# Optimization experiments

Hardware: AMD Instinct MI355X
Metric: run time of the kernel (lower is better)

Reference implementation:

```python
import jax, jax.numpy as jnp
import numpy as np

LSH_NUM_PROJS = 7
BLOCK_SIZE = 256      # key block size
SAMPLE_SIZE = 256
B, H, N, D = 1, 32, 8192, 128


def _gray_perm(num_projs):
    # AngularLSH._unit_hamming_distance_array: Gray-code bucket permutation
    a = np.array([0, 1], dtype=np.int32)
    for _ in range(num_projs - 1):
        a = np.concatenate([a, np.flip(a) + a.shape[0]])
    return jnp.asarray(a)


def _lsh_hash(x, proj_dir, perm):
    # x: [B,H,N,D], proj_dir: [D,R] -> bucket ids [B,H,N]
    bits = jnp.einsum('bhnd,dr->bhnr', x, proj_dir) > 0
    enc = 2 ** jnp.arange(proj_dir.shape[-1], dtype=jnp.int32)
    bin_ids = jnp.sum(bits.astype(jnp.int32) * enc, axis=-1)
    return perm[bin_ids]


def _attn_lse(q, k, v, scale, bias=None):
    # exact attention returning output and log-sum-exp of scaled scores
    s = jnp.einsum('...qd,...kd->...qk', q, k) * scale
    if bias is not None:
        s = s + bias
    m = jnp.max(s, axis=-1, keepdims=True)
    p = jnp.exp(s - m)
    denom = jnp.sum(p, axis=-1, keepdims=True)
    attn = jnp.einsum('...qk,...kd->...qd', p, v) / denom
    lse = m + jnp.log(denom)  # [..., q, 1]
    return attn, lse


def _take(x, idx):
    # gather along the sequence axis (dim 2); idx: [B,H,M]
    return jnp.take_along_axis(x, idx[..., None], axis=2)


def hyper_attention(q, k, v, proj_dir, sampled_set):
    b, h, n, d = q.shape
    scale = d ** -0.5
    perm = _gray_perm(LSH_NUM_PROJS)
    # 1) sortLSH: sort q and k by angular-LSH bucket (stable)
    q_idx = jnp.argsort(_lsh_hash(q, proj_dir, perm), axis=2)
    k_idx = jnp.argsort(_lsh_hash(k, proj_dir, perm), axis=2)
    q_idx_inv = jnp.argsort(q_idx, axis=2)
    q_s = _take(q, q_idx)
    k_s = _take(k, k_idx)
    v_s = _take(v, k_idx)
    nb = n // BLOCK_SIZE          # number of key blocks
    qbs = n // nb                 # query block size
    # block-diagonal exact attention in sorted order
    qb = q_s.reshape(b, h, nb, qbs, d)
    kb = k_s.reshape(b, h, nb, BLOCK_SIZE, d)
    vb = v_s.reshape(b, h, nb, BLOCK_SIZE, d)
    attn_blk, lse_blk = _attn_lse(qb, kb, vb, scale)
    attn_blk = attn_blk.reshape(b, h, n, d)
    lse_blk = lse_blk.reshape(b, h, n, 1)
    attn_blk = _take(attn_blk, q_idx_inv)
    lse_blk = _take(lse_blk, q_idx_inv)
    # 2) residual: uniform sampling of keys (indices into sorted key order)
    s_size = sampled_set.shape[-1]
    k_sub = _take(k_s, sampled_set)   # [B,H,S,D]
    v_sub = _take(v_s, sampled_set)
    # mask out samples falling in the query's own diagonal block
    same_block = (jnp.arange(n)[None, None, :, None] // qbs) == (sampled_set[:, :, None, :] // BLOCK_SIZE)
    bias = jnp.where(same_block, jnp.finfo(q.dtype).min, 0.0).astype(q.dtype)
    attn_res, lse_res = _attn_lse(q_s, k_sub, v_sub, scale, bias=bias)
    lse_res = lse_res + jnp.log(n / s_size)  # importance weight n_key/sample_size
    attn_res = _take(attn_res, q_idx_inv)
    lse_res = _take(lse_res, q_idx_inv)
    # 3) combine estimators: softmax-weighted average in log space
    lse = jnp.logaddexp(lse_blk, lse_res)
    return jnp.exp(lse_blk - lse) * attn_blk + jnp.exp(lse_res - lse) * attn_res


def setup_inputs() -> dict:
    key = jax.random.key(0)
    k1, k2, k3, k4, k5 = jax.random.split(key, 5)
    return {
        'queries': jax.random.normal(k1, (B, H, N, D), dtype=jnp.float32),
        'keys': jax.random.normal(k2, (B, H, N, D), dtype=jnp.float32),
        'vals': jax.random.normal(k3, (B, H, N, D), dtype=jnp.float32),
        'proj_dir': jax.random.normal(k4, (D, LSH_NUM_PROJS), dtype=jnp.float32),
        'sampled_set': jax.random.randint(k5, (B, H, SAMPLE_SIZE), 0, N),
    }


def reference(queries, keys, vals, proj_dir, sampled_set):
    return hyper_attention(queries, keys, vals, proj_dir, sampled_set)
```

## Files before the change

kernel.cpp:

```cpp
#include <hip/hip_runtime.h>
#include <hip/hip_bf16.h>
#include <math.h>

#define Hh 32
#define Nseq 8192
#define Dh 128
#define NBd 32
#define BLKSZ 256
#define SAMP 256
#define CHK 64
#define NCH 8
#define LOG32 3.4657359027997265f
#define SCALE 0.088388347648318447f
#define SKW 136
#define SVW 72

typedef float f32x4 __attribute__((ext_vector_type(4)));
typedef unsigned ui32x4 __attribute__((ext_vector_type(4)));
typedef __bf16 bf16x8 __attribute__((ext_vector_type(8)));

__device__ __forceinline__ f32x4 mfma16(bf16x8 a, bf16x8 b, f32x4 c) {
  return __builtin_amdgcn_mfma_f32_16x16x32_bf16(a, b, c, 0, 0, 0);
}

__device__ __forceinline__ bf16x8 cvt8(const float* __restrict__ p) {
  float4 a = ((const float4*)p)[0];
  float4 b = ((const float4*)p)[1];
  bf16x8 r;
  r[0] = (__bf16)a.x; r[1] = (__bf16)a.y; r[2] = (__bf16)a.z; r[3] = (__bf16)a.w;
  r[4] = (__bf16)b.x; r[5] = (__bf16)b.y; r[6] = (__bf16)b.z; r[7] = (__bf16)b.w;
  return r;
}

__device__ __forceinline__ bf16x8 cvt8v(float4 a, float4 b) {
  bf16x8 r;
  r[0] = (__bf16)a.x; r[1] = (__bf16)a.y; r[2] = (__bf16)a.z; r[3] = (__bf16)a.w;
  r[4] = (__bf16)b.x; r[5] = (__bf16)b.y; r[6] = (__bf16)b.z; r[7] = (__bf16)b.w;
  return r;
}

__device__ __forceinline__ unsigned packv(float a, float b) {
  __bf16 ba = (__bf16)a, bb = (__bf16)b;
  return ((unsigned)__builtin_bit_cast(unsigned short, bb) << 16) |
         (unsigned)__builtin_bit_cast(unsigned short, ba);
}

__device__ __forceinline__ unsigned pack2(float a, float b, float& ra, float& rb) {
  __bf16 ba = (__bf16)a, bb = (__bf16)b;
  ra = (float)ba; rb = (float)bb;
  return ((unsigned)__builtin_bit_cast(unsigned short, bb) << 16) |
         (unsigned)__builtin_bit_cast(unsigned short, ba);
}

__global__ __launch_bounds__(256) void lsh_hash_kernel(
    const float* __restrict__ q, const float* __restrict__ k,
    const float* __restrict__ proj, int* __restrict__ buckets) {
  int row = blockIdx.x * 256 + threadIdx.x;
  const float* x = ((row >> 18) ? k : q) + (size_t)(row & (Hh * Nseq - 1)) * Dh;
  double acc[7] = {0, 0, 0, 0, 0, 0, 0};
#pragma unroll 8
  for (int d0 = 0; d0 < Dh; d0 += 4) {
    float4 xv = *(const float4*)(x + d0);
    double x0 = (double)xv.x, x1 = (double)xv.y, x2 = (double)xv.z, x3 = (double)xv.w;
#pragma unroll
    for (int j = 0; j < 7; j++) {
      acc[j] = fma(x0, (double)proj[(d0 + 0) * 7 + j], acc[j]);
      acc[j] = fma(x1, (double)proj[(d0 + 1) * 7 + j], acc[j]);
      acc[j] = fma(x2, (double)proj[(d0 + 2) * 7 + j], acc[j]);
      acc[j] = fma(x3, (double)proj[(d0 + 3) * 7 + j], acc[j]);
    }
  }
  int bin = 0;
#pragma unroll
  for (int j = 0; j < 7; j++) bin |= (acc[j] > 0.0 ? 1 : 0) << j;
  buckets[row] = bin ^ (bin >> 1);
}

__global__ __launch_bounds__(256) void bucket_sort_kernel(
    const int* __restrict__ buckets, int* __restrict__ idx) {
  __shared__ unsigned short hist[256][128];
  __shared__ unsigned btot[128];
  __shared__ unsigned wsum[2];
  const int t = threadIdx.x;
  const int base = blockIdx.x * Nseq;

  {
    uint4* h4 = (uint4*)&hist[0][0];
#pragma unroll
    for (int j = 0; j < 16; j++) h4[t + j * 256] = uint4{0, 0, 0, 0};
  }
  __syncthreads();

  int bloc[32];
#pragma unroll 8
  for (int i = 0; i < 32; i++) {
    int b = buckets[base + t * 32 + i];
    bloc[i] = b;
    hist[t][b]++;
  }
  __syncthreads();

  unsigned v = 0;
  if (t < 128) {
    unsigned run = 0;
    for (int cch = 0; cch < 256; cch++) {
      unsigned h = hist[cch][t];
      hist[cch][t] = (unsigned short)run;
      run += h;
    }
    btot[t] = run;
    v = run;
  }
  __syncthreads();

  unsigned sc = v;
  if (t < 128) {
#pragma unroll
    for (int s = 1; s < 64; s <<= 1) {
      unsigned u = __shfl_up(sc, s);
      if ((t & 63) >= s) sc += u;
    }
    if ((t & 63) == 63) wsum[t >> 6] = sc;
  }
  __syncthreads();
  if (t < 128) {
    unsigned excl = sc - v + ((t >> 6) ? wsum[0] : 0u);
    btot[t] = excl;
  }
  __syncthreads();
  if (t < 128) {
    unsigned short e = (unsigned short)btot[t];
    for (int cch = 0; cch < 256; cch++) hist[cch][t] += e;
  }
  __syncthreads();

#pragma unroll 8
  for (int i = 0; i < 32; i++) {
    int b = bloc[i];
    unsigned pos = hist[t][b]++;
    idx[base + pos] = t * 32 + i;
  }
}

__global__ __launch_bounds__(256) void permute_samp_kernel(
    const float* __restrict__ k, const float* __restrict__ v,
    const int* __restrict__ k_idx, const int* __restrict__ sampled,
    __bf16* __restrict__ K_sp, __bf16* __restrict__ V_sp) {
  __shared__ __attribute__((aligned(16))) __bf16 s_t[Dh][SVW];
  const int tile = blockIdx.x, bh = blockIdx.y;
  const int t = threadIdx.x;
  const int j = t >> 2, seg = (t & 3) * 32;
  const int dpos = tile * 64 + j;
  const int sp = sampled[bh * SAMP + dpos];
  const int orig = k_idx[bh * Nseq + sp];
  {
    const float4* kp = (const float4*)(k + ((size_t)bh * Nseq + orig) * Dh + seg);
    __bf16* dst = K_sp + ((size_t)bh * SAMP + dpos) * Dh + seg;
#pragma unroll
    for (int i = 0; i < 4; i++) *(bf16x8*)(dst + i * 8) = cvt8v(kp[2 * i], kp[2 * i + 1]);
  }
  {
    const float4* vp = (const float4*)(v + ((size_t)bh * Nseq + orig) * Dh + seg);
#pragma unroll
    for (int i = 0; i < 8; i++) {
      float4 a = vp[i];
      s_t[seg + i * 4 + 0][j] = (__bf16)a.x;
      s_t[seg + i * 4 + 1][j] = (__bf16)a.y;
      s_t[seg + i * 4 + 2][j] = (__bf16)a.z;
      s_t[seg + i * 4 + 3][j] = (__bf16)a.w;
    }
  }
  __syncthreads();
  {
    int d = t >> 1, half = (t & 1) * 32;
    __bf16* dst = V_sp + ((size_t)(bh * Dh + d)) * SAMP + tile * 64 + half;
    const __bf16* srcp = &s_t[d][half];
#pragma unroll
    for (int i = 0; i < 4; i++) *(ui32x4*)(dst + i * 8) = *(const ui32x4*)(srcp + i * 8);
  }
}

__global__ __launch_bounds__(512, 2) void hyper_attn_kernel(
    const float* __restrict__ q, const float* __restrict__ k, const float* __restrict__ v,
    const __bf16* __restrict__ K_sp, const __bf16* __restrict__ V_sp,
    const int* __restrict__ sampled, const int* __restrict__ q_idx,
    const int* __restrict__ k_idx, float* __restrict__ out) {
  __shared__ int s_orig[BLKSZ];
  __shared__ __attribute__((aligned(16))) float s_add[SAMP];
  __shared__ __attribute__((aligned(16))) __bf16 s_k[2][CHK][SKW];
  __shared__ __attribute__((aligned(16))) __bf16 s_vt[2][Dh][SVW];

  const int c = blockIdx.x, bh = blockIdx.y;
  const int tid = threadIdx.x;
  const int w = tid >> 6, l = tid & 63;
  const int l4 = l >> 4, lm = l & 15;
  const int jk = tid >> 3, pk = tid & 7;
  const int dv = tid >> 2, ks = (tid & 3) * 16;
  const int kb = (tid & 31) * 2, dg = tid >> 5;

  {
    int jj = tid;
    if (jj < BLKSZ) {
      s_orig[jj] = k_idx[bh * Nseq + c * BLKSZ + jj];
    } else {
      int sp = sampled[bh * SAMP + (jj - BLKSZ)];
      s_add[jj - BLKSZ] = ((sp >> 8) == c) ? -1e38f : LOG32;
    }
  }

  bf16x8 qf[2][4];
  const int* qi = q_idx + bh * Nseq + c * BLKSZ + w * 32;
#pragma unroll
  for (int rt = 0; rt < 2; rt++) {
    int orig = qi[rt * 16 + lm];
    const float* qp = q + ((size_t)bh * Nseq + orig) * Dh + l4 * 8;
#pragma unroll
    for (int dc = 0; dc < 4; dc++) qf[rt][dc] = cvt8(qp + dc * 32);
  }

  f32x4 O[2][8];
  float mrow[2] = {-INFINITY, -INFINITY};
  float lsum[2] = {0.f, 0.f};
#pragma unroll
  for (int rt = 0; rt < 2; rt++)
#pragma unroll
    for (int dt = 0; dt < 8; dt++) { O[rt][dt][0]=0.f; O[rt][dt][1]=0.f; O[rt][dt][2]=0.f; O[rt][dt][3]=0.f; }

  __syncthreads();

  {
    int origk = s_orig[jk];
    const float* kp = k + ((size_t)bh * Nseq + origk) * Dh + pk * 16;
    *(bf16x8*)&s_k[0][jk][pk * 16]     = cvt8(kp);
    *(bf16x8*)&s_k[0][jk][pk * 16 + 8] = cvt8(kp + 8);
    int ra = s_orig[kb], rb = s_orig[kb + 1];
    const float4* va = (const float4*)(v + ((size_t)bh * Nseq + ra) * Dh + dg * 8);
    const float4* vb = (const float4*)(v + ((size_t)bh * Nseq + rb) * Dh + dg * 8);
    float4 A0 = va[0], A1 = va[1], B0 = vb[0], B1 = vb[1];
    float ta[8] = {A0.x,A0.y,A0.z,A0.w,A1.x,A1.y,A1.z,A1.w};
    float tb[8] = {B0.x,B0.y,B0.z,B0.w,B1.x,B1.y,B1.z,B1.w};
#pragma unroll
    for (int dd = 0; dd < 8; dd++)
      *(unsigned*)&s_vt[0][dg * 8 + dd][kb] = packv(ta[dd], tb[dd]);
  }
  __syncthreads();

  const int laneA = lm + 32 * (l4 & 1);
  const bool hi = (l4 >> 1) & 1;

  for (int ch = 0; ch < NCH; ch++) {
    const int cur = ch & 1;
    const int cn = ch + 1;
    const bool pfg = (cn < 4);
    const bool pfc = (cn >= 4 && cn < NCH);

    float4 kA, kB, kC, kD, vA0, vA1, vB0, vB1;
    ui32x4 ksA, ksB, vsA, vsB;
    if (pfg) {
      int origk = s_orig[cn * CHK + jk];
      const float4* kp = (const float4*)(k + ((size_t)bh * Nseq + origk) * Dh + pk * 16);
      kA = kp[0]; kB = kp[1]; kC = kp[2]; kD = kp[3];
      int ra = s_orig[cn * CHK + kb], rb = s_orig[cn * CHK + kb + 1];
      const float4* va = (const float4*)(v + ((size_t)bh * Nseq + ra) * Dh + dg * 8);
      const float4* vb = (const float4*)(v + ((size_t)bh * Nseq + rb) * Dh + dg * 8);
      vA0 = va[0]; vA1 = va[1]; vB0 = vb[0]; vB1 = vb[1];
    } else if (pfc) {
      const __bf16* kp = K_sp + ((size_t)(bh * SAMP + (cn - 4) * CHK + jk)) * Dh + pk * 16;
      ksA = *(const ui32x4*)kp; ksB = *(const ui32x4*)(kp + 8);
      const __bf16* vp = V_sp + ((size_t)(bh * Dh + dv)) * SAMP + (cn - 4) * CHK + ks;
      vsA = *(const ui32x4*)vp; vsB = *(const ui32x4*)(vp + 8);
    }
    __builtin_amdgcn_sched_barrier(0);

    float sc[2][4][4];
    __builtin_amdgcn_s_setprio(1);
#pragma unroll
    for (int ct = 0; ct < 4; ct++) {
      f32x4 acc0, acc1;
      acc0[0]=0.f;acc0[1]=0.f;acc0[2]=0.f;acc0[3]=0.f;
      acc1[0]=0.f;acc1[1]=0.f;acc1[2]=0.f;acc1[3]=0.f;
#pragma unroll
      for (int dc = 0; dc < 4; dc++) {
        bf16x8 kf = *(const bf16x8*)&s_k[cur][ct * 16 + lm][dc * 32 + l4 * 8];
        acc0 = mfma16(kf, qf[0][dc], acc0);
        acc1 = mfma16(kf, qf[1][dc], acc1);
      }
      f32x4 addv;
      if (ch < 4) { addv[0]=0.f; addv[1]=0.f; addv[2]=0.f; addv[3]=0.f; }
      else addv = *(const f32x4*)&s_add[(ch - 4) * CHK + ct * 16 + l4 * 4];
#pragma unroll
      for (int r = 0; r < 4; r++) {
        sc[0][ct][r] = acc0[r] * SCALE + addv[r];
        sc[1][ct][r] = acc1[r] * SCALE + addv[r];
      }
    }
    __builtin_amdgcn_s_setprio(0);

    unsigned q01[2][4], q23[2][4];
#pragma unroll
    for (int rt = 0; rt < 2; rt++) {
      float mc = sc[rt][0][0];
#pragma unroll
      for (int ct = 0; ct < 4; ct++)
#pragma unroll
        for (int r = 0; r < 4; r++) mc = fmaxf(mc, sc[rt][ct][r]);
      mc = fmaxf(mc, __shfl_xor(mc, 16));
      mc = fmaxf(mc, __shfl_xor(mc, 32));
      float mn = fmaxf(mrow[rt], mc);
      float alpha = __expf(mrow[rt] - mn);
      mrow[rt] = mn;
      f32x4 aO;
#pragma unroll
      for (int r = 0; r < 4; r++) aO[r] = __shfl(alpha, l4 * 4 + r);
#pragma unroll
      for (int dt = 0; dt < 8; dt++) O[rt][dt] *= aO;
      float rsum = 0.f;
#pragma unroll
      for (int ct = 0; ct < 4; ct++) {
        float p0 = __expf(sc[rt][ct][0] - mn);
        float p1 = __expf(sc[rt][ct][1] - mn);
        float p2 = __expf(sc[rt][ct][2] - mn);
        float p3 = __expf(sc[rt][ct][3] - mn);
        float ra, rb, rc, rd;
        q01[rt][ct] = pack2(p0, p1, ra, rb);
        q23[rt][ct] = pack2(p2, p3, rc, rd);
        rsum += (ra + rb) + (rc + rd);
      }
      rsum += __shfl_xor(rsum, 16);
      rsum += __shfl_xor(rsum, 32);
      lsum[rt] = lsum[rt] * alpha + rsum;
    }

    if (pfg) {
      *(bf16x8*)&s_k[cur ^ 1][jk][pk * 16]     = cvt8v(kA, kB);
      *(bf16x8*)&s_k[cur ^ 1][jk][pk * 16 + 8] = cvt8v(kC, kD);
      float ta[8] = {vA0.x,vA0.y,vA0.z,vA0.w,vA1.x,vA1.y,vA1.z,vA1.w};
      float tb[8] = {vB0.x,vB0.y,vB0.z,vB0.w,vB1.x,vB1.y,vB1.z,vB1.w};
#pragma unroll
      for (int dd = 0; dd < 8; dd++)
        *(unsigned*)&s_vt[cur ^ 1][dg * 8 + dd][kb] = packv(ta[dd], tb[dd]);
    } else if (pfc) {
      *(ui32x4*)&s_k[cur ^ 1][jk][pk * 16]     = ksA;
      *(ui32x4*)&s_k[cur ^ 1][jk][pk * 16 + 8] = ksB;
      *(ui32x4*)&s_vt[cur ^ 1][dv][ks]     = vsA;
      *(ui32x4*)&s_vt[cur ^ 1][dv][ks + 8] = vsB;
    }

    __builtin_amdgcn_s_setprio(1);
#pragma unroll
    for (int kc = 0; kc < 2; kc++) {
      bf16x8 pa[2];
#pragma unroll
      for (int rt = 0; rt < 2; rt++) {
        unsigned a0 = __shfl((int)q01[rt][2 * kc],     laneA);
        unsigned b0 = __shfl((int)q01[rt][2 * kc + 1], laneA);
        unsigned a1 = __shfl((int)q23[rt][2 * kc],     laneA);
        unsigned b1 = __shfl((int)q23[rt][2 * kc + 1], laneA);
        unsigned a2 = __shfl((int)q01[rt][2 * kc],     laneA + 16);
        unsigned b2 = __shfl((int)q01[rt][2 * kc + 1], laneA + 16);
        unsigned a3 = __shfl((int)q23[rt][2 * kc],     laneA + 16);
        unsigned b3 = __shfl((int)q23[rt][2 * kc + 1], laneA + 16);
        ui32x4 pw;
        pw[0] = hi ? b0 : a0;
        pw[1] = hi ? b1 : a1;
        pw[2] = hi ? b2 : a2;
        pw[3] = hi ? b3 : a3;
        pa[rt] = __builtin_bit_cast(bf16x8, pw);
      }
#pragma unroll
      for (int dt = 0; dt < 8; dt++) {
        bf16x8 vb = *(const bf16x8*)&s_vt[cur][dt * 16 + lm][kc * 32 + l4 * 8];
        O[0][dt] = mfma16(pa[0], vb, O[0][dt]);
        O[1][dt] = mfma16(pa[1], vb, O[1][dt]);
      }
    }
    __builtin_amdgcn_s_setprio(0);
    __syncthreads();
  }

#pragma unroll
  for (int rt = 0; rt < 2; rt++) {
    float inv = 1.0f / lsum[rt];
    f32x4 invr;
#pragma unroll
    for (int r = 0; r < 4; r++) invr[r] = __shfl(inv, l4 * 4 + r);
#pragma unroll
    for (int r = 0; r < 4; r++) {
      int orow = q_idx[bh * Nseq + c * BLKSZ + w * 32 + rt * 16 + l4 * 4 + r];
      float* op = out + ((size_t)bh * Nseq + orow) * Dh + lm;
#pragma unroll
      for (int dt = 0; dt < 8; dt++) op[dt * 16] = O[rt][dt][r] * invr[r];
    }
  }
}

extern "C" void kernel_launch(void* const* d_in, const int* in_sizes, int n_in,
                              void* d_out, int out_size, void* d_ws, size_t ws_size,
                              hipStream_t stream) {
  const float* q    = (const float*)d_in[0];
  const float* k    = (const float*)d_in[1];
  const float* v    = (const float*)d_in[2];
  const float* proj = (const float*)d_in[3];
  const int* samp   = (const int*)d_in[4];
  float* out = (float*)d_out;

  int* buckets = (int*)d_ws;
  int* idx = buckets + 2 * Hh * Nseq;
  __bf16* K_sp = (__bf16*)(idx + 2 * Hh * Nseq);
  __bf16* V_sp = K_sp + (size_t)Hh * SAMP * Dh;

  lsh_hash_kernel<<<(2 * Hh * Nseq) / 256, 256, 0, stream>>>(q, k, proj, buckets);
  bucket_sort_kernel<<<2 * Hh, 256, 0, stream>>>(buckets, idx);
  permute_samp_kernel<<<dim3(4, Hh), 256, 0, stream>>>(
      k, v, idx + Hh * Nseq , samp, K_sp, V_sp);
  hyper_attn_kernel<<<dim3(NBd, Hh), 512, 0, stream>>>(
      q, k, v, K_sp, V_sp, samp, idx , idx + Hh * Nseq , out);
}
```

Measured before the change: 267.2 us.

## Read sampled K/V fragments directly from global memory instead of LDS staging

Splits the chunk loop into two phases. The block-diagonal phase keeps LDS double buffering, with four chunks now instead of eight. The residual-sample phase loads pre-converted bf16 K_sp/V_sp MFMA fragments straight from global (L2-resident) memory with no LDS writes or __syncthreads. This is meant to remove LDS staging and barrier cost for the shared sample keys. The trade-off is more scattered global reads per wave and no prefetch overlap in the second phase.

```diff
diff --git a/kernel.cpp b/kernel.cpp
--- a/kernel.cpp
+++ b/kernel.cpp
@@ -9,7 +9,6 @@
 #define BLKSZ 256
 #define SAMP 256
 #define CHK 64
-#define NCH 8
 #define LOG32 3.4657359027997265f
 #define SCALE 0.088388347648318447f
 #define SKW 136
@@ -195,7 +194,6 @@
   const int w = tid >> 6, l = tid & 63;
   const int l4 = l >> 4, lm = l & 15;
   const int jk = tid >> 3, pk = tid & 7;
-  const int dv = tid >> 2, ks = (tid & 3) * 16;
   const int kb = (tid & 31) * 2, dg = tid >> 5;
 
   {
@@ -248,27 +246,19 @@
   const int laneA = lm + 32 * (l4 & 1);
   const bool hi = (l4 >> 1) & 1;
 
-  for (int ch = 0; ch < NCH; ch++) {
+  for (int ch = 0; ch < 4; ch++) {
     const int cur = ch & 1;
-    const int cn = ch + 1;
-    const bool pfg = (cn < 4);
-    const bool pfc = (cn >= 4 && cn < NCH);
+    const bool pfg = (ch < 3);
 
     float4 kA, kB, kC, kD, vA0, vA1, vB0, vB1;
-    ui32x4 ksA, ksB, vsA, vsB;
     if (pfg) {
-      int origk = s_orig[cn * CHK + jk];
+      int origk = s_orig[(ch + 1) * CHK + jk];
       const float4* kp = (const float4*)(k + ((size_t)bh * Nseq + origk) * Dh + pk * 16);
       kA = kp[0]; kB = kp[1]; kC = kp[2]; kD = kp[3];
-      int ra = s_orig[cn * CHK + kb], rb = s_orig[cn * CHK + kb + 1];
+      int ra = s_orig[(ch + 1) * CHK + kb], rb = s_orig[(ch + 1) * CHK + kb + 1];
       const float4* va = (const float4*)(v + ((size_t)bh * Nseq + ra) * Dh + dg * 8);
       const float4* vb = (const float4*)(v + ((size_t)bh * Nseq + rb) * Dh + dg * 8);
       vA0 = va[0]; vA1 = va[1]; vB0 = vb[0]; vB1 = vb[1];
-    } else if (pfc) {
-      const __bf16* kp = K_sp + ((size_t)(bh * SAMP + (cn - 4) * CHK + jk)) * Dh + pk * 16;
-      ksA = *(const ui32x4*)kp; ksB = *(const ui32x4*)(kp + 8);
-      const __bf16* vp = V_sp + ((size_t)(bh * Dh + dv)) * SAMP + (cn - 4) * CHK + ks;
-      vsA = *(const ui32x4*)vp; vsB = *(const ui32x4*)(vp + 8);
     }
     __builtin_amdgcn_sched_barrier(0);
 
@@ -285,13 +275,10 @@
         acc0 = mfma16(kf, qf[0][dc], acc0);
         acc1 = mfma16(kf, qf[1][dc], acc1);
       }
-      f32x4 addv;
-      if (ch < 4) { addv[0]=0.f; addv[1]=0.f; addv[2]=0.f; addv[3]=0.f; }
-      else addv = *(const f32x4*)&s_add[(ch - 4) * CHK + ct * 16 + l4 * 4];
 #pragma unroll
       for (int r = 0; r < 4; r++) {
-        sc[0][ct][r] = acc0[r] * SCALE + addv[r];
-        sc[1][ct][r] = acc1[r] * SCALE + addv[r];
+        sc[0][ct][r] = acc0[r] * SCALE;
+        sc[1][ct][r] = acc1[r] * SCALE;
       }
     }
     __builtin_amdgcn_s_setprio(0);
@@ -339,11 +326,6 @@
 #pragma unroll
       for (int dd = 0; dd < 8; dd++)
         *(unsigned*)&s_vt[cur ^ 1][dg * 8 + dd][kb] = packv(ta[dd], tb[dd]);
-    } else if (pfc) {
-      *(ui32x4*)&s_k[cur ^ 1][jk][pk * 16]     = ksA;
-      *(ui32x4*)&s_k[cur ^ 1][jk][pk * 16 + 8] = ksB;
-      *(ui32x4*)&s_vt[cur ^ 1][dv][ks]     = vsA;
-      *(ui32x4*)&s_vt[cur ^ 1][dv][ks + 8] = vsB;
     }
 
     __builtin_amdgcn_s_setprio(1);
@@ -375,7 +357,98 @@
       }
     }
     __builtin_amdgcn_s_setprio(0);
-    __syncthreads();
+    if (ch < 3) __syncthreads();
+  }
+
+  for (int ch = 0; ch < 4; ch++) {
+    const __bf16* Kb = K_sp + ((size_t)(bh * SAMP + ch * CHK)) * Dh;
+    const __bf16* Vb = V_sp + ((size_t)bh * Dh) * SAMP + ch * CHK;
+
+    float sc[2][4][4];
+#pragma unroll
+    for (int ct = 0; ct < 4; ct++) {
+      bf16x8 kfr[4];
+#pragma unroll
+      for (int dc = 0; dc < 4; dc++)
+        kfr[dc] = *(const bf16x8*)(Kb + (size_t)(ct * 16 + lm) * Dh + dc * 32 + l4 * 8);
+      f32x4 acc0, acc1;
+      acc0[0]=0.f;acc0[1]=0.f;acc0[2]=0.f;acc0[3]=0.f;
+      acc1[0]=0.f;acc1[1]=0.f;acc1[2]=0.f;acc1[3]=0.f;
+#pragma unroll
+      for (int dc = 0; dc < 4; dc++) {
+        acc0 = mfma16(kfr[dc], qf[0][dc], acc0);
+        acc1 = mfma16(kfr[dc], qf[1][dc], acc1);
+      }
+      f32x4 addv = *(const f32x4*)&s_add[ch * CHK + ct * 16 + l4 * 4];
+#pragma unroll
+      for (int r = 0; r < 4; r++) {
+        sc[0][ct][r] = acc0[r] * SCALE + addv[r];
+        sc[1][ct][r] = acc1[r] * SCALE + addv[r];
+      }
+    }
+
+    unsigned q01[2][4], q23[2][4];
+#pragma unroll
+    for (int rt = 0; rt < 2; rt++) {
+      float mc = sc[rt][0][0];
+#pragma unroll
+      for (int ct = 0; ct < 4; ct++)
+#pragma unroll
+        for (int r = 0; r < 4; r++) mc = fmaxf(mc, sc[rt][ct][r]);
+      mc = fmaxf(mc, __shfl_xor(mc, 16));
+      mc = fmaxf(mc, __shfl_xor(mc, 32));
+      float mn = fmaxf(mrow[rt], mc);
+      float alpha = __expf(mrow[rt] - mn);
+      mrow[rt] = mn;
+      f32x4 aO;
+#pragma unroll
+      for (int r = 0; r < 4; r++) aO[r] = __shfl(alpha, l4 * 4 + r);
+#pragma unroll
+      for (int dt = 0; dt < 8; dt++) O[rt][dt] *= aO;
+      float rsum = 0.f;
+#pragma unroll
+      for (int ct = 0; ct < 4; ct++) {
+        float p0 = __expf(sc[rt][ct][0] - mn);
+        float p1 = __expf(sc[rt][ct][1] - mn);
+        float p2 = __expf(sc[rt][ct][2] - mn);
+        float p3 = __expf(sc[rt][ct][3] - mn);
+        float ra, rb, rc, rd;
+        q01[rt][ct] = pack2(p0, p1, ra, rb);
+        q23[rt][ct] = pack2(p2, p3, rc, rd);
+        rsum += (ra + rb) + (rc + rd);
+      }
+      rsum += __shfl_xor(rsum, 16);
+      rsum += __shfl_xor(rsum, 32);
+      lsum[rt] = lsum[rt] * alpha + rsum;
+    }
+
+#pragma unroll
+    for (int kc = 0; kc < 2; kc++) {
+      bf16x8 pa[2];
+#pragma unroll
+      for (int rt = 0; rt < 2; rt++) {
+        unsigned a0 = __shfl((int)q01[rt][2 * kc],     laneA);
+        unsigned b0 = __shfl((int)q01[rt][2 * kc + 1], laneA);
+        unsigned a1 = __shfl((int)q23[rt][2 * kc],     laneA);
+        unsigned b1 = __shfl((int)q23[rt][2 * kc + 1], laneA);
+        unsigned a2 = __shfl((int)q01[rt][2 * kc],     laneA + 16);
+        unsigned b2 = __shfl((int)q01[rt][2 * kc + 1], laneA + 16);
+        unsigned a3 = __shfl((int)q23[rt][2 * kc],     laneA + 16);
+        unsigned b3 = __shfl((int)q23[rt][2 * kc + 1], laneA + 16);
+        ui32x4 pw;
+        pw[0] = hi ? b0 : a0;
+        pw[1] = hi ? b1 : a1;
+        pw[2] = hi ? b2 : a2;
+        pw[3] = hi ? b3 : a3;
+        pa[rt] = __builtin_bit_cast(bf16x8, pw);
+      }
+#pragma unroll
+      for (int dt = 0; dt < 8; dt++) {
+        bf16x8 vb = *(const bf16x8*)(Vb + (size_t)(dt * 16 + lm) * SAMP + kc * 32 + l4 * 8);
+        O[0][dt] = mfma16(pa[0], vb, O[0][dt]);
+        O[1][dt] = mfma16(pa[1], vb, O[1][dt]);
+      }
+    }
   }
 
 #pragma unroll
```

Measured after the change: 324.5 us. 21.5% more time.
